# Optimization experiments

Hardware: AMD Instinct MI355X
Metric: run time of the kernel (lower is better)

The kernel has to match this reference:

```python
import jax, jax.numpy as jnp
import numpy as np

B, T, CIN = 32, 4096, 165
CH, RCH, EDIM, NEMB = 256, 32, 64, 512


def setup_inputs() -> dict:
    key = jax.random.key(0)
    ks = iter(jax.random.split(key, 40))

    def w(o, i):
        return jax.random.normal(next(ks), (o, i), jnp.float32) * (1.0 / np.sqrt(i))

    def b(o):
        return jnp.zeros((o,), jnp.float32)

    inp = {"x": jax.random.normal(next(ks), (B, T, CIN), jnp.float32)}
    # Encoder: conv(165->128), relu, conv(128->256), relu, conv(256->256), 2 resblocks, relu
    inp["enc_w0"], inp["enc_b0"] = w(CH // 2, CIN), b(CH // 2)
    inp["enc_w1"], inp["enc_b1"] = w(CH, CH // 2), b(CH)
    inp["enc_w2"], inp["enc_b2"] = w(CH, CH), b(CH)
    inp["er0_w0"], inp["er0_b0"] = w(RCH, CH), b(RCH)
    inp["er0_w1"], inp["er0_b1"] = w(CH, RCH), b(CH)
    inp["er1_w0"], inp["er1_b0"] = w(RCH, CH), b(RCH)
    inp["er1_w1"], inp["er1_b1"] = w(CH, RCH), b(CH)
    # quantize_conv (256->64)
    inp["qc_w"], inp["qc_b"] = w(EDIM, CH), b(EDIM)
    # codebook [dim, n_embed]
    inp["embed"] = jax.random.normal(next(ks), (EDIM, NEMB), jnp.float32)
    # Decoder: conv(64->256), 2 resblocks, relu, conv(256->128), relu, conv(128->165)
    inp["dec_w0"], inp["dec_b0"] = w(CH, EDIM), b(CH)
    inp["dr0_w0"], inp["dr0_b0"] = w(RCH, CH), b(RCH)
    inp["dr0_w1"], inp["dr0_b1"] = w(CH, RCH), b(CH)
    inp["dr1_w0"], inp["dr1_b0"] = w(RCH, CH), b(RCH)
    inp["dr1_w1"], inp["dr1_b1"] = w(CH, RCH), b(CH)
    inp["dec_w1"], inp["dec_b1"] = w(CH // 2, CH), b(CH // 2)
    inp["dec_w2"], inp["dec_b2"] = w(CIN, CH // 2), b(CIN)
    return inp


def _conv(h, w, bb):
    # 1x1 Conv1d == pointwise matmul over channels; h: [B,C_in,T]
    return jnp.einsum('oi,bit->bot', w, h) + bb[None, :, None]


def _res(h, w0, b0, w1, b1):
    # Sequential(ReLU, Conv, ReLU, Conv) with residual add
    return h + _conv(jax.nn.relu(_conv(jax.nn.relu(h), w0, b0)), w1, b1)


def reference(x, enc_w0, enc_b0, enc_w1, enc_b1, enc_w2, enc_b2,
              er0_w0, er0_b0, er0_w1, er0_b1, er1_w0, er1_b0, er1_w1, er1_b1,
              qc_w, qc_b, embed,
              dec_w0, dec_b0, dr0_w0, dr0_b0, dr0_w1, dr0_b1,
              dr1_w0, dr1_b0, dr1_w1, dr1_b1, dec_w1, dec_b1, dec_w2, dec_b2):
    h = jnp.transpose(x, (0, 2, 1))  # [B,CIN,T]
    # Encoder
    h = _conv(h, enc_w0, enc_b0)
    h = jax.nn.relu(h)
    h = _conv(h, enc_w1, enc_b1)
    h = jax.nn.relu(h)
    h = _conv(h, enc_w2, enc_b2)
    h = _res(h, er0_w0, er0_b0, er0_w1, er0_b1)
    h = _res(h, er1_w0, er1_b0, er1_w1, er1_b1)
    h = jax.nn.relu(h)
    # quantize_conv + permute to [B,T,D]
    z = jnp.transpose(_conv(h, qc_w, qc_b), (0, 2, 1))
    # Quantize (eval mode: no EMA buffer updates)
    flat = z.reshape(-1, EDIM)  # [N,D]
    dist = (flat ** 2).sum(1, keepdims=True) - 2.0 * (flat @ embed) + (embed ** 2).sum(0, keepdims=True)  # [N,NEMB]
    ind = jnp.argmin(dist, axis=1)
    quant = embed.T[ind].reshape(z.shape)  # [B,T,D]
    diff = jnp.mean((jax.lax.stop_gradient(quant) - z) ** 2)[None]  # shape (1,)
    quant = z + jax.lax.stop_gradient(quant - z)  # straight-through
    # Decoder
    h = jnp.transpose(quant, (0, 2, 1))  # [B,D,T]
    h = _conv(h, dec_w0, dec_b0)
    h = _res(h, dr0_w0, dr0_b0, dr0_w1, dr0_b1)
    h = _res(h, dr1_w0, dr1_b0, dr1_w1, dr1_b1)
    h = jax.nn.relu(h)
    h = _conv(h, dec_w1, dec_b1)
    h = jax.nn.relu(h)
    h = _conv(h, dec_w2, dec_b2)
    dec = jnp.transpose(h, (0, 2, 1))  # [B,T,CIN]
    return dec, diff
```

## Files before the change

### kernel.cpp

```cpp
#include <hip/hip_runtime.h>
#include <hip/hip_bf16.h>


#define NTOT 131072
#define EDIM 64
#define NEMB 512

__global__ void detect_k(const void* __restrict__ x, int* __restrict__ flag,
                         float* __restrict__ acc)
{
    __shared__ int s_bad;
    if (threadIdx.x == 0) s_bad = 0;
    __syncthreads();
    const unsigned short* u = (const unsigned short*)x;
    int bad = 0;
    for (int i = threadIdx.x; i < 2048; i += 256) {
        unsigned short h = u[i];
        int ex = (h >> 7) & 0xFF;
        if (h != 0 && (ex < 100 || ex > 140)) bad++;
    }
    atomicAdd(&s_bad, bad);
    __syncthreads();
    if (threadIdx.x == 0) { *flag = (s_bad > 256) ? 1 : 0; *acc = 0.f; }
}

struct WTbl { const void* p[31]; int off[31]; int n[31]; int Kd[31]; };

__global__ void convw_k(WTbl t, float* __restrict__ dst, const int* __restrict__ flag)
{
    const bool f32 = (*flag != 0);
    const int ti = blockIdx.x;
    const void* src = t.p[ti];
    float* d = dst + t.off[ti];
    const int n = t.n[ti];
    const int K = t.Kd[ti];
    if (K == 0) {
        for (int i = threadIdx.x; i < n; i += 256)
            d[i] = f32 ? ((const float*)src)[i]
                       : __bfloat162float(((const __hip_bfloat16*)src)[i]);
    } else {
        const int O = n / K;
        for (int j = threadIdx.x; j < n; j += 256) {
            int k = j / O, o = j - k * O;
            int si = o * K + k;
            d[j] = f32 ? ((const float*)src)[si]
                       : __bfloat162float(((const __hip_bfloat16*)src)[si]);
        }
    }
}

__global__ __launch_bounds__(256)
void enc01_k(const void* __restrict__ X,
             const float* __restrict__ W0t, const float* __restrict__ B0,
             const float* __restrict__ W1t, const float* __restrict__ B1,
             float* __restrict__ Y, const int* __restrict__ dtf)
{
    __shared__ float S[64][132];

    const bool f32d = (*dtf != 0);
    const int tid = threadIdx.x;
    const int r0  = blockIdx.x * 64;

    const int tx = tid & 15;
    const int ty = tid >> 4;

    float acc1[4][8] = {};
    for (int h = 0; h < 2; ++h) {
        const int kb = h * 84;
        for (int e = tid; e < 64 * 84; e += 256) {
            int m = e / 84, k = e - m * 84;
            int kg = kb + k;
            float v = 0.f;
            if (kg < 165) {
                size_t gi = (size_t)(r0 + m) * 165 + kg;
                v = f32d ? ((const float*)X)[gi]
                         : __bfloat162float(((const __hip_bfloat16*)X)[gi]);
            }
            S[m][k] = v;
        }
        __syncthreads();

        for (int k4 = 0; k4 < 84; k4 += 4) {
            float a4[4][4];
            #pragma unroll
            for (int i = 0; i < 4; ++i)
                *(float4*)&a4[i][0] = *(const float4*)&S[ty * 4 + i][k4];
            const int kwb = kb + k4;
            #pragma unroll
            for (int kk = 0; kk < 4; ++kk) {
                float b[8];
                *(float4*)&b[0] = *(const float4*)(W0t + (size_t)(kwb + kk) * 128 + tx * 4);
                *(float4*)&b[4] = *(const float4*)(W0t + (size_t)(kwb + kk) * 128 + 64 + tx * 4);
                #pragma unroll
                for (int i = 0; i < 4; ++i)
                    #pragma unroll
                    for (int j = 0; j < 8; ++j)
                        acc1[i][j] = fmaf(a4[i][kk], b[j], acc1[i][j]);
            }
        }
        __syncthreads();
    }

    {
        float bb[8];
        *(float4*)&bb[0] = *(const float4*)(B0 + tx * 4);
        *(float4*)&bb[4] = *(const float4*)(B0 + 64 + tx * 4);
        #pragma unroll
        for (int i = 0; i < 4; ++i) {
            float4 v0, v1;
            v0.x = fmaxf(acc1[i][0] + bb[0], 0.f);
            v0.y = fmaxf(acc1[i][1] + bb[1], 0.f);
            v0.z = fmaxf(acc1[i][2] + bb[2], 0.f);
            v0.w = fmaxf(acc1[i][3] + bb[3], 0.f);
            v1.x = fmaxf(acc1[i][4] + bb[4], 0.f);
            v1.y = fmaxf(acc1[i][5] + bb[5], 0.f);
            v1.z = fmaxf(acc1[i][6] + bb[6], 0.f);
            v1.w = fmaxf(acc1[i][7] + bb[7], 0.f);
            *(float4*)&S[ty * 4 + i][tx * 4]      = v0;
            *(float4*)&S[ty * 4 + i][64 + tx * 4] = v1;
        }
    }
    __syncthreads();

    const int tx2 = tid & 31;
    const int ty2 = tid >> 5;
    float acc2[2][8][4] = {};
    for (int k4 = 0; k4 < 128; k4 += 4) {
        float a4[8][4];
        #pragma unroll
        for (int i = 0; i < 8; ++i)
            *(float4*)&a4[i][0] = *(const float4*)&S[ty2 * 8 + i][k4];
        #pragma unroll
        for (int kk = 0; kk < 4; ++kk) {
            float b0[4], b1[4];
            *(float4*)&b0[0] = *(const float4*)(W1t + (size_t)(k4 + kk) * 256 + tx2 * 4);
            *(float4*)&b1[0] = *(const float4*)(W1t + (size_t)(k4 + kk) * 256 + 128 + tx2 * 4);
            #pragma unroll
            for (int i = 0; i < 8; ++i)
                #pragma unroll
                for (int j = 0; j < 4; ++j) {
                    acc2[0][i][j] = fmaf(a4[i][kk], b0[j], acc2[0][i][j]);
                    acc2[1][i][j] = fmaf(a4[i][kk], b1[j], acc2[1][i][j]);
                }
        }
    }
    {
        float bb0[4], bb1[4];
        *(float4*)&bb0[0] = *(const float4*)(B1 + tx2 * 4);
        *(float4*)&bb1[0] = *(const float4*)(B1 + 128 + tx2 * 4);
        #pragma unroll
        for (int i = 0; i < 8; ++i) {
            const size_t row = (size_t)(r0 + ty2 * 8 + i) * 256;
            float4 v0, v1;
            v0.x = fmaxf(acc2[0][i][0] + bb0[0], 0.f);
            v0.y = fmaxf(acc2[0][i][1] + bb0[1], 0.f);
            v0.z = fmaxf(acc2[0][i][2] + bb0[2], 0.f);
            v0.w = fmaxf(acc2[0][i][3] + bb0[3], 0.f);
            v1.x = fmaxf(acc2[1][i][0] + bb1[0], 0.f);
            v1.y = fmaxf(acc2[1][i][1] + bb1[1], 0.f);
            v1.z = fmaxf(acc2[1][i][2] + bb1[2], 0.f);
            v1.w = fmaxf(acc2[1][i][3] + bb1[3], 0.f);
            *(float4*)(Y + row + tx2 * 4)       = v0;
            *(float4*)(Y + row + 128 + tx2 * 4) = v1;
        }
    }
}

__global__ __launch_bounds__(256)
void res_k(float* __restrict__ H,
           const float* __restrict__ W0t, const float* __restrict__ B0,
           const float* __restrict__ W1t, const float* __restrict__ B1)
{
    __shared__ float Hr[64][260];
    __shared__ float T1[32][68];

    const int tid = threadIdx.x;
    const int r0  = blockIdx.x * 64;

    #pragma unroll
    for (int it = 0; it < 16; ++it) {
        int idx = tid + it * 256;
        int q = idx & 63, m = idx >> 6;
        float4 v = *(const float4*)(H + (size_t)(r0 + m) * 256 + q * 4);
        *(float4*)&Hr[m][q * 4] = v;
    }
    __syncthreads();

    const int tx1 = tid & 7;
    const int ty1 = tid >> 3;
    float acc1[2][4] = {};
    #pragma unroll 8
    for (int k = 0; k < 256; ++k) {
        float b[4];
        *(float4*)&b[0] = *(const float4*)(W0t + (size_t)k * 32 + tx1 * 4);
        float a0 = fmaxf(Hr[ty1 * 2][k], 0.f);
        float a1 = fmaxf(Hr[ty1 * 2 + 1][k], 0.f);
        #pragma unroll
        for (int j = 0; j < 4; ++j) {
            acc1[0][j] = fmaf(a0, b[j], acc1[0][j]);
            acc1[1][j] = fmaf(a1, b[j], acc1[1][j]);
        }
    }
    {
        float bb[4];
        *(float4*)&bb[0] = *(const float4*)(B0 + tx1 * 4);
        #pragma unroll
        for (int i = 0; i < 2; ++i)
            #pragma unroll
            for (int j = 0; j < 4; ++j)
                T1[tx1 * 4 + j][ty1 * 2 + i] = fmaxf(acc1[i][j] + bb[j], 0.f);
    }
    __syncthreads();

    const int tx2 = tid & 31;
    const int ty2 = tid >> 5;
    float acc2[2][8][4] = {};
    #pragma unroll 8
    for (int k = 0; k < 32; ++k) {
        float b0[4], b1[4], a[8];
        *(float4*)&b0[0] = *(const float4*)(W1t + (size_t)k * 256 + tx2 * 4);
        *(float4*)&b1[0] = *(const float4*)(W1t + (size_t)k * 256 + 128 + tx2 * 4);
        *(float4*)&a[0] = *(const float4*)&T1[k][ty2 * 8];
        *(float4*)&a[4] = *(const float4*)&T1[k][ty2 * 8 + 4];
        #pragma unroll
        for (int i = 0; i < 8; ++i)
            #pragma unroll
            for (int j = 0; j < 4; ++j) {
                acc2[0][i][j] = fmaf(a[i], b0[j], acc2[0][i][j]);
                acc2[1][i][j] = fmaf(a[i], b1[j], acc2[1][i][j]);
            }
    }
    {
        float bb0[4], bb1[4];
        *(float4*)&bb0[0] = *(const float4*)(B1 + tx2 * 4);
        *(float4*)&bb1[0] = *(const float4*)(B1 + 128 + tx2 * 4);
        #pragma unroll
        for (int i = 0; i < 8; ++i) {
            const int row = ty2 * 8 + i;
            const size_t gr = (size_t)(r0 + row) * 256;
            float4 h0 = *(const float4*)&Hr[row][tx2 * 4];
            float4 h1 = *(const float4*)&Hr[row][128 + tx2 * 4];
            float4 v0, v1;
            v0.x = h0.x + acc2[0][i][0] + bb0[0];
            v0.y = h0.y + acc2[0][i][1] + bb0[1];
            v0.z = h0.z + acc2[0][i][2] + bb0[2];
            v0.w = h0.w + acc2[0][i][3] + bb0[3];
            v1.x = h1.x + acc2[1][i][0] + bb1[0];
            v1.y = h1.y + acc2[1][i][1] + bb1[1];
            v1.z = h1.z + acc2[1][i][2] + bb1[2];
            v1.w = h1.w + acc2[1][i][3] + bb1[3];
            *(float4*)(H + gr + tx2 * 4)       = v0;
            *(float4*)(H + gr + 128 + tx2 * 4) = v1;
        }
    }
}

template <int K, int OC, bool PRE_RELU, bool POST_RELU>
__global__ __launch_bounds__(256)
void gemmf_k(const float* __restrict__ X, const float* __restrict__ Wt,
             const float* __restrict__ Bv, float* __restrict__ Y)
{
    constexpr int KH  = (K < 128) ? K : 128;
    constexpr int SW  = KH + 4;
    constexpr int TX  = (OC == 256) ? 32 : 16;
    constexpr int TYN = 256 / TX;
    constexpr int RP  = 64 / TYN;
    constexpr int NCH = (OC > TX * 4) ? 2 : 1;
    constexpr int CHW = OC / NCH;

    __shared__ float S[64 * SW];

    const int tid = threadIdx.x;
    const int r0  = blockIdx.x * 64;
    const int tx  = tid & (TX - 1);
    const int ty  = tid / TX;

    float acc[NCH][RP][4] = {};
    float4 bA[4][NCH], bB[4][NCH];

#define LOADW(dst, kb)                                                        \
    {                                                                         \
        _Pragma("unroll")                                                     \
        for (int kk = 0; kk < 4; ++kk)                                        \
            _Pragma("unroll")                                                 \
            for (int c = 0; c < NCH; ++c)                                     \
                dst[kk][c] = *(const float4*)(Wt + (size_t)((kb) + kk) * OC   \
                                              + c * CHW + tx * 4);            \
    }

#define COMPQ(bsrc, kl)                                                       \
    {                                                                         \
        float a4[RP][4];                                                      \
        _Pragma("unroll")                                                     \
        for (int i = 0; i < RP; ++i)                                          \
            *(float4*)&a4[i][0] = *(const float4*)&S[(ty * RP + i) * SW + (kl)]; \
        _Pragma("unroll")                                                     \
        for (int kk = 0; kk < 4; ++kk)                                        \
            _Pragma("unroll")                                                 \
            for (int c = 0; c < NCH; ++c) {                                   \
                const float* bp = (const float*)&bsrc[kk][c];                 \
                _Pragma("unroll")                                             \
                for (int i = 0; i < RP; ++i)                                  \
                    _Pragma("unroll")                                         \
                    for (int j = 0; j < 4; ++j)                               \
                        acc[c][i][j] = fmaf(a4[i][kk], bp[j], acc[c][i][j]);  \
            }                                                                 \
    }

    LOADW(bA, 0);

    for (int h = 0; h < K; h += KH) {
        #pragma unroll
        for (int it = 0; it < (64 * KH / 4) / 256; ++it) {
            int idx = tid + it * 256;
            int m = idx / (KH / 4), g = idx % (KH / 4);
            float4 v = *(const float4*)(X + (size_t)(r0 + m) * K + h + g * 4);
            if (PRE_RELU) {
                v.x = fmaxf(v.x, 0.f); v.y = fmaxf(v.y, 0.f);
                v.z = fmaxf(v.z, 0.f); v.w = fmaxf(v.w, 0.f);
            }
            *(float4*)&S[m * SW + g * 4] = v;
        }
        __syncthreads();

        for (int k8 = 0; k8 < KH; k8 += 8) {
            LOADW(bB, h + k8 + 4);
            COMPQ(bA, k8);
            const int kn = (h + k8 + 8 < K) ? (h + k8 + 8) : 0;
            LOADW(bA, kn);
            COMPQ(bB, k8 + 4);
        }
        __syncthreads();
    }
#undef LOADW
#undef COMPQ

    #pragma unroll
    for (int c = 0; c < NCH; ++c) {
        float bb[4];
        *(float4*)&bb[0] = *(const float4*)(Bv + c * CHW + tx * 4);
        #pragma unroll
        for (int i = 0; i < RP; ++i) {
            float4 v;
            v.x = acc[c][i][0] + bb[0];
            v.y = acc[c][i][1] + bb[1];
            v.z = acc[c][i][2] + bb[2];
            v.w = acc[c][i][3] + bb[3];
            if (POST_RELU) {
                v.x = fmaxf(v.x, 0.f); v.y = fmaxf(v.y, 0.f);
                v.z = fmaxf(v.z, 0.f); v.w = fmaxf(v.w, 0.f);
            }
            *(float4*)(Y + (size_t)(r0 + ty * RP + i) * OC + c * CHW + tx * 4) = v;
        }
    }
}

template <bool PRE_RELU, bool POST_RELU, int YM>
__global__ __launch_bounds__(256)
void gemm_k(const float* __restrict__ X, const float* __restrict__ Wt,
            const float* __restrict__ Bv, void* __restrict__ Y,
            int K, int O, const int* __restrict__ dtf)
{
    __shared__ float Xs[32][132];
    __shared__ float Ws[32][68];

    const bool f32d = (YM == 1) ? (*dtf != 0) : false;
    const int tid = threadIdx.x;
    const int tx  = tid & 15;
    const int ty  = tid >> 4;
    const int o0  = blockIdx.x * 64;
    const int m0  = blockIdx.y * 128;

    float acc[8][4] = {};
    const int KC = K >> 5;
    for (int kc = 0; kc < KC; ++kc) {
        const int k0 = kc << 5;
        #pragma unroll
        for (int it = 0; it < 4; ++it) {
            int idx = tid + it * 256;
            int kq = idx & 7, m = idx >> 3;
            float4 v = *(const float4*)(X + (size_t)(m0 + m) * K + k0 + kq * 4);
            if (PRE_RELU) {
                v.x = fmaxf(v.x, 0.f); v.y = fmaxf(v.y, 0.f);
                v.z = fmaxf(v.z, 0.f); v.w = fmaxf(v.w, 0.f);
            }
            Xs[kq * 4 + 0][m] = v.x; Xs[kq * 4 + 1][m] = v.y;
            Xs[kq * 4 + 2][m] = v.z; Xs[kq * 4 + 3][m] = v.w;
        }
        #pragma unroll
        for (int it = 0; it < 8; ++it) {
            int e = tid + it * 256;
            int kk = e & 31, o = e >> 5;
            int og = o0 + o;
            Ws[kk][o] = (og < O) ? Wt[(size_t)(k0 + kk) * O + og] : 0.f;
        }
        __syncthreads();
        #pragma unroll
        for (int kk = 0; kk < 32; ++kk) {
            float a[8], b[4];
            *(float4*)&a[0] = *(const float4*)&Xs[kk][ty * 8];
            *(float4*)&a[4] = *(const float4*)&Xs[kk][ty * 8 + 4];
            *(float4*)&b[0] = *(const float4*)&Ws[kk][tx * 4];
            #pragma unroll
            for (int i = 0; i < 8; ++i)
                #pragma unroll
                for (int j = 0; j < 4; ++j)
                    acc[i][j] = fmaf(a[i], b[j], acc[i][j]);
        }
        __syncthreads();
    }

    #pragma unroll
    for (int j = 0; j < 4; ++j) {
        int c = o0 + tx * 4 + j;
        if (c >= O) continue;
        float bb = Bv[c];
        #pragma unroll
        for (int i = 0; i < 8; ++i) {
            int r = m0 + ty * 8 + i;
            float v = acc[i][j] + bb;
            if (POST_RELU) v = fmaxf(v, 0.f);
            size_t yi = (size_t)r * O + c;
            if (YM == 0)   ((float*)Y)[yi] = v;
            else if (f32d) ((float*)Y)[yi] = v;
            else           ((__hip_bfloat16*)Y)[yi] = __float2bfloat16(v);
        }
    }
}

__global__ void prep_k(const float* __restrict__ E, float* __restrict__ Et)
{
    int idx = blockIdx.x * 256 + threadIdx.x;
    Et[(idx & 511) * EDIM + (idx >> 9)] = E[idx];
}

__global__ void e2_k(const float* __restrict__ Et, float* __restrict__ e2)
{
    int e = blockIdx.x * 256 + threadIdx.x;
    float s = 0.f;
    #pragma unroll
    for (int d = 0; d < EDIM; ++d) { float v = Et[e * EDIM + d]; s = fmaf(v, v, s); }
    e2[e] = s;
}

__global__ __launch_bounds__(256)
void vq_k(float* __restrict__ Zq, const float* __restrict__ Ed,
          const float* __restrict__ Et, const float* __restrict__ e2,
          float* __restrict__ acc)
{
    __shared__ float Zs[64][132];
    __shared__ float Es[64][68];

    const int tid = threadIdx.x;
    const int tx  = tid & 15;
    const int ty  = tid >> 4;
    const int r0  = blockIdx.x * 128;

    #pragma unroll
    for (int it = 0; it < 8; ++it) {
        int idx = tid + it * 256;
        int dq = idx & 15, m = idx >> 4;
        float4 v = *(const float4*)(Zq + (size_t)(r0 + m) * 64 + dq * 4);
        Zs[dq * 4 + 0][m] = v.x; Zs[dq * 4 + 1][m] = v.y;
        Zs[dq * 4 + 2][m] = v.z; Zs[dq * 4 + 3][m] = v.w;
    }

    float best[8];
    int   bi[8];
    #pragma unroll
    for (int i = 0; i < 8; ++i) { best[i] = 3.4e38f; bi[i] = 0; }

    for (int cc = 0; cc < 8; ++cc) {
        const int c0 = cc * 64;
        #pragma unroll
        for (int it = 0; it < 4; ++it) {
            int idx = tid + it * 256;
            int oq = idx & 15, kk = idx >> 4;
            *(float4*)&Es[kk][oq * 4] =
                *(const float4*)(Ed + (size_t)kk * NEMB + c0 + oq * 4);
        }
        float4 e2v = *(const float4*)(e2 + c0 + tx * 4);
        __syncthreads();

        float a4[8][4] = {};
        #pragma unroll 8
        for (int kk = 0; kk < 64; ++kk) {
            float a[8], b[4];
            *(float4*)&a[0] = *(const float4*)&Zs[kk][ty * 8];
            *(float4*)&a[4] = *(const float4*)&Zs[kk][ty * 8 + 4];
            *(float4*)&b[0] = *(const float4*)&Es[kk][tx * 4];
            #pragma unroll
            for (int i = 0; i < 8; ++i)
                #pragma unroll
                for (int j = 0; j < 4; ++j)
                    a4[i][j] = fmaf(a[i], b[j], a4[i][j]);
        }

        const float e2a[4] = {e2v.x, e2v.y, e2v.z, e2v.w};
        #pragma unroll
        for (int j = 0; j < 4; ++j) {
            const int code = c0 + tx * 4 + j;
            #pragma unroll
            for (int i = 0; i < 8; ++i) {
                float s = fmaf(-2.f, a4[i][j], e2a[j]);
                if (s < best[i]) { best[i] = s; bi[i] = code; }
            }
        }
        __syncthreads();
    }

    #pragma unroll
    for (int i = 0; i < 8; ++i) {
        #pragma unroll
        for (int m = 1; m < 16; m <<= 1) {
            float ob = __shfl_xor(best[i], m);
            int   oi = __shfl_xor(bi[i], m);
            if (ob < best[i] || (ob == best[i] && oi < bi[i])) {
                best[i] = ob; bi[i] = oi;
            }
        }
    }

    float ds = 0.f;
    #pragma unroll
    for (int i = 0; i < 8; ++i) {
        const int row = r0 + ty * 8 + i;
        float4 qv = *(const float4*)(Et + (size_t)bi[i] * 64 + tx * 4);
        float* zp = Zq + (size_t)row * 64 + tx * 4;
        float4 zv = *(const float4*)zp;
        float t;
        t = qv.x - zv.x; ds = fmaf(t, t, ds);
        t = qv.y - zv.y; ds = fmaf(t, t, ds);
        t = qv.z - zv.z; ds = fmaf(t, t, ds);
        t = qv.w - zv.w; ds = fmaf(t, t, ds);
        *(float4*)zp = qv;
    }
    #pragma unroll
    for (int off = 32; off; off >>= 1) ds += __shfl_down(ds, off);
    if ((tid & 63) == 0) atomicAdd(acc, ds);
}

__global__ void diff_k(const float* __restrict__ acc, void* __restrict__ out,
                       size_t off, const int* __restrict__ dtf)
{
    if (threadIdx.x == 0) {
        float v = *acc * (1.0f / 8388608.0f);
        if (*dtf) ((float*)out)[off] = v;
        else      ((__hip_bfloat16*)out)[off] = __float2bfloat16(v);
    }
}

extern "C" void kernel_launch(void* const* d_in, const int* in_sizes, int n_in,
                              void* d_out, int out_size, void* d_ws, size_t ws_size,
                              hipStream_t stream)
{
    const size_t MB = 1048576;
    char* ws = (char*)d_ws;
    float* Zq  = (float*)ws;
    float* A1  = (float*)(ws + 32 * MB);
    float* A2  = (float*)(ws + 32 * MB + 128 * MB);
    float* Wf  = (float*)(ws + 288 * MB);
    float* Et  = (float*)(ws + 288 * MB + 1310720);
    float* e2  = Et + NEMB * EDIM;
    float* acc = e2 + NEMB;
    int*   dtf = (int*)(acc + 1);

    static const int KDIM[32] = {0, 165,0, 128,0, 256,0, 256,0, 32,0, 256,0, 32,0,
                                 256,0, 0, 64,0, 256,0, 32,0, 256,0, 32,0, 256,0, 128,0};
    WTbl t;
    int off[32];
    int cum = 0;
    for (int i = 1; i < 32; ++i) {
        t.p[i - 1]   = d_in[i];
        t.off[i - 1] = cum;
        t.n[i - 1]   = in_sizes[i];
        t.Kd[i - 1]  = KDIM[i];
        off[i] = cum;
        cum += in_sizes[i];
    }
    const float* W_ew0 = Wf + off[1],  *B_ew0 = Wf + off[2];
    const float* W_ew1 = Wf + off[3],  *B_ew1 = Wf + off[4];
    const float* W_ew2 = Wf + off[5],  *B_ew2 = Wf + off[6];
    const float* W_r0a = Wf + off[7],  *B_r0a = Wf + off[8];
    const float* W_r0b = Wf + off[9],  *B_r0b = Wf + off[10];
    const float* W_r1a = Wf + off[11], *B_r1a = Wf + off[12];
    const float* W_r1b = Wf + off[13], *B_r1b = Wf + off[14];
    const float* W_qc  = Wf + off[15], *B_qc  = Wf + off[16];
    const float* Emb   = Wf + off[17];
    const float* W_d0  = Wf + off[18], *B_d0  = Wf + off[19];
    const float* W_s0a = Wf + off[20], *B_s0a = Wf + off[21];
    const float* W_s0b = Wf + off[22], *B_s0b = Wf + off[23];
    const float* W_s1a = Wf + off[24], *B_s1a = Wf + off[25];
    const float* W_s1b = Wf + off[26], *B_s1b = Wf + off[27];
    const float* W_d1  = Wf + off[28], *B_d1  = Wf + off[29];
    const float* W_d2  = Wf + off[30], *B_d2  = Wf + off[31];

    dim3 blk(256);
    const int NB = NTOT / 64;

    detect_k<<<1, blk, 0, stream>>>(d_in[0], dtf, acc);
    convw_k<<<31, blk, 0, stream>>>(t, Wf, dtf);
    prep_k<<<128, blk, 0, stream>>>(Emb, Et);
    e2_k<<<2, blk, 0, stream>>>(Et, e2);

    enc01_k<<<NB, blk, 0, stream>>>(d_in[0], W_ew0, B_ew0, W_ew1, B_ew1, A1, dtf);
    gemmf_k<256, 256, false, false><<<NB, blk, 0, stream>>>(A1, W_ew2, B_ew2, A2);
    res_k<<<NB, blk, 0, stream>>>(A2, W_r0a, B_r0a, W_r0b, B_r0b);
    res_k<<<NB, blk, 0, stream>>>(A2, W_r1a, B_r1a, W_r1b, B_r1b);
    gemmf_k<256, 64, true, false><<<NB, blk, 0, stream>>>(A2, W_qc, B_qc, Zq);

    vq_k<<<NTOT / 128, blk, 0, stream>>>(Zq, Emb, Et, e2, acc);

    gemmf_k<64, 256, false, false><<<NB, blk, 0, stream>>>(Zq, W_d0, B_d0, A1);
    res_k<<<NB, blk, 0, stream>>>(A1, W_s0a, B_s0a, W_s0b, B_s0b);
    res_k<<<NB, blk, 0, stream>>>(A1, W_s1a, B_s1a, W_s1b, B_s1b);
    gemmf_k<256, 128, true, true><<<NB, blk, 0, stream>>>(A1, W_d1, B_d1, A2);
    gemm_k<false, false, 1><<<dim3(3, NTOT / 128), blk, 0, stream>>>
        (A2, W_d2, B_d2, d_out, 128, 165, dtf);

    diff_k<<<1, 64, 0, stream>>>(acc, d_out, (size_t)NTOT * 165, dtf);
}
```

Measured before the change: 1.626 ms.

## Halve res_k shared memory by staging H in two K-halves and rereading residual

The residual-block kernel now stages the 64x256 input tile through a 64x128 shared buffer in two passes, roughly halving LDS use so more blocks can reside per CU. The first GEMM reads activations as float4 vectors from shared memory instead of scalars. Because the full tile is no longer kept, the residual add rereads H from global memory, which adds traffic and an extra barrier per half in exchange for higher occupancy.

```diff
diff --git a/kernel.cpp b/kernel.cpp
--- a/kernel.cpp
+++ b/kernel.cpp
@@ -171,36 +171,51 @@
            const float* __restrict__ W0t, const float* __restrict__ B0,
            const float* __restrict__ W1t, const float* __restrict__ B1)
 {
-    __shared__ float Hr[64][260];
+    __shared__ float S[64][132];
     __shared__ float T1[32][68];
 
     const int tid = threadIdx.x;
     const int r0  = blockIdx.x * 64;
-
-    #pragma unroll
-    for (int it = 0; it < 16; ++it) {
-        int idx = tid + it * 256;
-        int q = idx & 63, m = idx >> 6;
-        float4 v = *(const float4*)(H + (size_t)(r0 + m) * 256 + q * 4);
-        *(float4*)&Hr[m][q * 4] = v;
-    }
-    __syncthreads();
 
     const int tx1 = tid & 7;
     const int ty1 = tid >> 3;
     float acc1[2][4] = {};
-    #pragma unroll 8
-    for (int k = 0; k < 256; ++k) {
-        float b[4];
-        *(float4*)&b[0] = *(const float4*)(W0t + (size_t)k * 32 + tx1 * 4);
-        float a0 = fmaxf(Hr[ty1 * 2][k], 0.f);
-        float a1 = fmaxf(Hr[ty1 * 2 + 1][k], 0.f);
-        #pragma unroll
-        for (int j = 0; j < 4; ++j) {
-            acc1[0][j] = fmaf(a0, b[j], acc1[0][j]);
-            acc1[1][j] = fmaf(a1, b[j], acc1[1][j]);
-        }
-    }
+
+    for (int h = 0; h < 2; ++h) {
+        const int kb = h * 128;
+        #pragma unroll
+        for (int it = 0; it < 8; ++it) {
+            int idx = tid + it * 256;
+            int q = idx & 31, m = idx >> 5;
+            float4 v = *(const float4*)(H + (size_t)(r0 + m) * 256 + kb + q * 4);
+            *(float4*)&S[m][q * 4] = v;
+        }
+        __syncthreads();
+
+        for (int k4 = 0; k4 < 128; k4 += 4) {
+            float a0[4], a1[4];
+            *(float4*)&a0[0] = *(const float4*)&S[ty1 * 2][k4];
+            *(float4*)&a1[0] = *(const float4*)&S[ty1 * 2 + 1][k4];
+            #pragma unroll
+            for (int q = 0; q < 4; ++q) {
+                a0[q] = fmaxf(a0[q], 0.f);
+                a1[q] = fmaxf(a1[q], 0.f);
+            }
+            const int kw = kb + k4;
+            #pragma unroll
+            for (int kk = 0; kk < 4; ++kk) {
+                float b[4];
+                *(float4*)&b[0] = *(const float4*)(W0t + (size_t)(kw + kk) * 32 + tx1 * 4);
+                #pragma unroll
+                for (int j = 0; j < 4; ++j) {
+                    acc1[0][j] = fmaf(a0[kk], b[j], acc1[0][j]);
+                    acc1[1][j] = fmaf(a1[kk], b[j], acc1[1][j]);
+                }
+            }
+        }
+        __syncthreads();
+    }
+
     {
         float bb[4];
         *(float4*)&bb[0] = *(const float4*)(B0 + tx1 * 4);
@@ -238,8 +253,8 @@
         for (int i = 0; i < 8; ++i) {
             const int row = ty2 * 8 + i;
             const size_t gr = (size_t)(r0 + row) * 256;
-            float4 h0 = *(const float4*)&Hr[row][tx2 * 4];
-            float4 h1 = *(const float4*)&Hr[row][128 + tx2 * 4];
+            float4 h0 = *(const float4*)(H + gr + tx2 * 4);
+            float4 h1 = *(const float4*)(H + gr + 128 + tx2 * 4);
             float4 v0, v1;
             v0.x = h0.x + acc2[0][i][0] + bb0[0];
             v0.y = h0.y + acc2[0][i][1] + bb0[1];
```

Result: no change. 1.656 ms (+1.9%).
